# Kernel optimization log

Measured on AMD Instinct MI355X. Metric: run time of the kernel, lower is better.

Reference implementation:

```python
import jax, jax.numpy as jnp
import numpy as np

EPS = 1e-10


def setup_inputs() -> dict:
    key = jax.random.key(0)
    k1, k2 = jax.random.split(key)
    B, C, H, W = 8, 16, 256, 256
    x = jax.random.normal(k1, (B, C, H, W), dtype=jnp.float32)
    # grid_sample-style normalized coords in [-1, 1]
    inv_grid = jax.random.uniform(k2, (B, H, W, 2), dtype=jnp.float32, minval=-1.0, maxval=1.0)
    return {"x": x, "inv_grid": inv_grid}


def reference(x, inv_grid):
    B, C, Hin, Win = x.shape
    h, w = Hin, Win  # OH = OW = None -> output size equals input size

    g = (inv_grid + 1.0) * 0.5
    # coord 0 scaled by h, coord 1 by w, shifted by +1 (padding row/col), clamped
    ci = jnp.clip(g[..., 0] * h + 1.0, 0.0, h + 1 - 2 * EPS)
    cj = jnp.clip(g[..., 1] * w + 1.0, 0.0, w + 1 - 2 * EPS)
    i0 = jnp.floor(ci).astype(jnp.int32)  # coords >= 0 so floor == trunc (.long())
    j0 = jnp.floor(cj).astype(jnp.int32)

    # broadcast over channel dim (grid is shared across channels)
    ci_ = ci[:, None]
    cj_ = cj[:, None]
    i0_ = i0[:, None]
    j0_ = j0[:, None]

    bidx = jnp.arange(B)[:, None, None, None]
    cidx = jnp.arange(C)[None, :, None, None]

    A = jnp.zeros((B, C, h + 3, w + 3), dtype=x.dtype)
    for di in range(2):
        wi = jax.nn.relu(1.0 - jnp.abs(ci_ - (i0_ + di).astype(ci_.dtype)))
        for dj in range(2):
            wj = jax.nn.relu(1.0 - jnp.abs(cj_ - (j0_ + dj).astype(cj_.dtype)))
            # bilinear splat scatter-add of x * weight into the 4 corner cells
            A = A.at[bidx, cidx, i0_ + di, j0_ + dj].add(x * (wi * wj))
    return A[..., 1:h + 1, 1:w + 1]
```

## Files before the change

### kernel.cpp

```cpp
#include <hip/hip_runtime.h>
#include <hip/hip_fp16.h>
#include <stdint.h>

#define BB 8
#define CC 16
#define HH 256
#define WW 256
#define HW (HH * WW)
#define NSRC (BB * HW)
#define NBLK (NSRC / 256)
#define MAXSLOT 15
#define CNT_BYTES ((size_t)NSRC * 4)


__global__ __launch_bounds__(256) void pass1_bin(
    const float* __restrict__ inv_grid,
    uint32_t* __restrict__ counts,
    uint2* __restrict__ srcs)
{
    const int idx = blockIdx.x * 256 + threadIdx.x;
    const float2 g2 = ((const float2*)inv_grid)[idx];
    const float ci = fminf(fmaxf(fmaf((g2.x + 1.0f) * 0.5f, (float)HH, 1.0f), 0.0f), 257.0f);
    const float cj = fminf(fmaxf(fmaf((g2.y + 1.0f) * 0.5f, (float)WW, 1.0f), 0.0f), 257.0f);
    const int i0 = (int)floorf(ci);
    const int j0 = (int)floorf(cj);
    const float fi = ci - (float)i0;
    const float fj = cj - (float)j0;
    const int bi = i0 - 1, bj = j0 - 1;
    uint32_t meta = 0xFFFFFFFFu;
    if (((unsigned)bi < HH) & ((unsigned)bj < WW)) {
        const int b = idx >> 16;
        const uint32_t bin = (b << 16) | (bi << 8) | bj;
        const uint32_t slot = atomicAdd(&counts[bin], 1u);
        if (slot < MAXSLOT) meta = (bin << 4) | slot;
    }
    const uint32_t fi16 = (uint32_t)(fi * 65535.0f + 0.5f);
    const uint32_t fj16 = (uint32_t)(fj * 65535.0f + 0.5f);
    uint2 m; m.x = meta; m.y = fi16 | (fj16 << 16);
    srcs[idx] = m;
}

__global__ __launch_bounds__(256) void scanA(
    const uint32_t* __restrict__ counts,
    uint2* __restrict__ co,
    uint32_t* __restrict__ bsum)
{
    __shared__ uint32_t s[256];
    const int t = threadIdx.x;
    const int i = blockIdx.x * 256 + t;
    const uint32_t v = counts[i];
    s[t] = v;
    __syncthreads();
#pragma unroll
    for (int d = 1; d < 256; d <<= 1) {
        const uint32_t u = (t >= d) ? s[t - d] : 0u;
        __syncthreads();
        s[t] += u;
        __syncthreads();
    }
    uint2 e; e.x = v; e.y = s[t] - v;
    co[i] = e;
    if (t == 255) bsum[blockIdx.x] = s[255];
}

__global__ __launch_bounds__(1024) void scanB(uint32_t* __restrict__ bsum)
{
    __shared__ uint32_t s[1024];
    const int t = threadIdx.x;
    const uint32_t a  = bsum[2 * t];
    const uint32_t b2 = bsum[2 * t + 1];
    const uint32_t pair = a + b2;
    s[t] = pair;
    __syncthreads();
#pragma unroll
    for (int d = 1; d < 1024; d <<= 1) {
        const uint32_t u = (t >= d) ? s[t - d] : 0u;
        __syncthreads();
        s[t] += u;
        __syncthreads();
    }
    const uint32_t excl = s[t] - pair;
    bsum[2 * t]     = excl;
    bsum[2 * t + 1] = excl + a;
}

__global__ __launch_bounds__(256) void fill_records(
    const float* __restrict__ x,
    const uint2* __restrict__ srcs,
    const uint2* __restrict__ co,
    const uint32_t* __restrict__ bsum,
    uint32_t* __restrict__ ff,
    uint4* __restrict__ pl)
{
    const int idx = blockIdx.x * 256 + threadIdx.x;
    const uint2 m = srcs[idx];
    if (m.x == 0xFFFFFFFFu) return;
    const uint32_t bin  = m.x >> 4;
    const uint32_t slot = m.x & 15u;
    const uint32_t pos  = co[bin].y + bsum[bin >> 8] + slot;

    const int b = idx >> 16;
    const int p = idx & 0xFFFF;
    const float* xp = x + (((size_t)b * CC) << 16) + p;

    uint32_t h[8];
#pragma unroll
    for (int q = 0; q < 8; ++q) {
        const float v0 = xp[(size_t)(2 * q)     << 16];
        const float v1 = xp[(size_t)(2 * q + 1) << 16];
        const uint32_t h0 = (uint32_t)__half_as_ushort(__float2half_rn(v0));
        const uint32_t h1 = (uint32_t)__half_as_ushort(__float2half_rn(v1));
        h[q] = h0 | (h1 << 16);
    }
    ff[pos] = m.y;
    uint4 q0; q0.x = h[0]; q0.y = h[1]; q0.z = h[2]; q0.w = h[3];
    uint4 q1; q1.x = h[4]; q1.y = h[5]; q1.z = h[6]; q1.w = h[7];
    pl[(size_t)pos * 2]     = q0;
    pl[(size_t)pos * 2 + 1] = q1;
}

__global__ __launch_bounds__(256) void gather_csr(
    const uint2* __restrict__ co,
    const uint32_t* __restrict__ bsum,
    const uint32_t* __restrict__ ff,
    const uint4* __restrict__ pl,
    float* __restrict__ out)
{
    const int g   = blockIdx.x;
    const int b   = g & 7;
    const int seq = g >> 3;
    const int r   = ((seq >> 4) << 4) + (threadIdx.x >> 4);
    const int c   = ((seq & 15) << 4) + (threadIdx.x & 15);

    float acc[CC];
#pragma unroll
    for (int q = 0; q < CC; ++q) acc[q] = 0.0f;

#pragma unroll
    for (int di = 0; di < 2; ++di) {
        const int i0c = r + di;
        if (i0c < 1) continue;
#pragma unroll
        for (int dj = 0; dj < 2; ++dj) {
            const int j0c = c + dj;
            if (j0c < 1) continue;
            const uint32_t bin = (b << 16) | ((i0c - 1) << 8) | (j0c - 1);
            const uint2 e = co[bin];
            uint32_t cnt = e.x;
            if (cnt > MAXSLOT) cnt = MAXSLOT;
            const uint32_t off = e.y + bsum[bin >> 8];
            for (uint32_t k = 0; k < cnt; ++k) {
                const size_t pos = (size_t)(off + k);
                const uint32_t f2 = ff[pos];
                const float fi = (float)(f2 & 0xFFFFu) * (1.0f / 65535.0f);
                const float fj = (float)(f2 >> 16)     * (1.0f / 65535.0f);
                const float wi = di ? (1.0f - fi) : fi;
                const float wj = dj ? (1.0f - fj) : fj;
                const float w = wi * wj;
                const uint4 q0 = pl[pos * 2];
                const uint4 q1 = pl[pos * 2 + 1];
                const uint32_t hs[8] = {q0.x, q0.y, q0.z, q0.w, q1.x, q1.y, q1.z, q1.w};
#pragma unroll
                for (int q = 0; q < 8; ++q) {
                    const float v0 = __half2float(__ushort_as_half((unsigned short)(hs[q] & 0xFFFFu)));
                    const float v1 = __half2float(__ushort_as_half((unsigned short)(hs[q] >> 16)));
                    acc[2 * q]     += w * v0;
                    acc[2 * q + 1] += w * v1;
                }
            }
        }
    }

    float* op = out + (((size_t)(b * CC)) << 16) + (r << 8) + c;
#pragma unroll
    for (int q = 0; q < CC; ++q)
        op[(size_t)q << 16] = acc[q];
}

__global__ __launch_bounds__(256) void invgrid_scatter_direct(
    const float* __restrict__ x,
    const float* __restrict__ inv_grid,
    float* __restrict__ out)
{
    const int idx = blockIdx.x * 256 + threadIdx.x;
    const int b = idx >> 16;
    const float2 g2 = ((const float2*)inv_grid)[idx];
    const float ci = fminf(fmaxf(fmaf((g2.x + 1.0f) * 0.5f, (float)HH, 1.0f), 0.0f), 257.0f);
    const float cj = fminf(fmaxf(fmaf((g2.y + 1.0f) * 0.5f, (float)WW, 1.0f), 0.0f), 257.0f);
    const int i0 = (int)floorf(ci);
    const int j0 = (int)floorf(cj);
    const float wi0 = fmaxf(0.0f, 1.0f - fabsf(ci - (float)i0));
    const float wi1 = fmaxf(0.0f, 1.0f - fabsf(ci - (float)(i0 + 1)));
    const float wj0 = fmaxf(0.0f, 1.0f - fabsf(cj - (float)j0));
    const float wj1 = fmaxf(0.0f, 1.0f - fabsf(cj - (float)(j0 + 1)));
    const float w00 = wi0 * wj0, w01 = wi0 * wj1;
    const float w10 = wi1 * wj0, w11 = wi1 * wj1;
    const int r0 = i0 - 1, r1 = i0, c0 = j0 - 1, c1 = j0;
    const bool vr0 = (unsigned)r0 < HH, vr1 = (unsigned)r1 < HH;
    const bool vc0 = (unsigned)c0 < WW, vc1 = (unsigned)c1 < WW;
    const int o00 = r0 * WW + c0, o01 = r0 * WW + c1;
    const int o10 = r1 * WW + c0, o11 = r1 * WW + c1;
    const int p = idx & 0xFFFF;
    const float* xp = x + (size_t)b * CC * HW + p;
    float* op = out + (size_t)b * CC * HW;
#pragma unroll
    for (int cch = 0; cch < CC; ++cch) {
        const float xv = xp[(size_t)cch * HW];
        float* ob = op + (size_t)cch * HW;
        if (vr0 & vc0) atomicAdd(ob + o00, xv * w00);
        if (vr0 & vc1) atomicAdd(ob + o01, xv * w01);
        if (vr1 & vc0) atomicAdd(ob + o10, xv * w10);
        if (vr1 & vc1) atomicAdd(ob + o11, xv * w11);
    }
}

extern "C" void kernel_launch(void* const* d_in, const int* in_sizes, int n_in,
                              void* d_out, int out_size, void* d_ws, size_t ws_size,
                              hipStream_t stream) {
    const float* x        = (const float*)d_in[0];
    const float* inv_grid = (const float*)d_in[1];
    float* out            = (float*)d_out;

    const size_t A = 256;
    size_t o_counts = 0;
    size_t o_co     = o_counts + (CNT_BYTES + A - 1) / A * A;
    size_t o_bsum   = o_co     + ((size_t)NSRC * 8 + A - 1) / A * A;
    size_t o_srcs   = o_bsum   + ((size_t)NBLK * 4 + A - 1) / A * A;
    size_t o_ff     = o_srcs   + ((size_t)NSRC * 8 + A - 1) / A * A;
    size_t o_pl     = o_ff     + (CNT_BYTES + A - 1) / A * A;
    size_t need     = o_pl     + (size_t)NSRC * 32;

    if (ws_size >= need) {
        char* w = (char*)d_ws;
        uint32_t* counts = (uint32_t*)(w + o_counts);
        uint2*    co     = (uint2*)   (w + o_co);
        uint32_t* bsum   = (uint32_t*)(w + o_bsum);
        uint2*    srcs   = (uint2*)   (w + o_srcs);
        uint32_t* ff     = (uint32_t*)(w + o_ff);
        uint4*    pl     = (uint4*)   (w + o_pl);
        hipMemsetAsync(counts, 0, CNT_BYTES, stream);
        pass1_bin   <<<NBLK, 256,  0, stream>>>(inv_grid, counts, srcs);
        scanA       <<<NBLK, 256,  0, stream>>>(counts, co, bsum);
        scanB       <<<1,    1024, 0, stream>>>(bsum);
        fill_records<<<NBLK, 256,  0, stream>>>(x, srcs, co, bsum, ff, pl);
        gather_csr  <<<NBLK, 256,  0, stream>>>(co, bsum, ff, pl, out);
    } else {
        hipMemsetAsync(d_out, 0, (size_t)out_size * sizeof(float), stream);
        invgrid_scatter_direct<<<NBLK, 256, 0, stream>>>(x, inv_grid, out);
    }
}
```

Measured before the change: 155.8 us.

## Replace two-level scan with atomic-cursor wave scan and flatten gather loop

The block-wide shared-memory scan plus the single-block scanB kernel are replaced by a wavefront shuffle scan whose block base comes from an atomicAdd on a global cursor, which removes one kernel launch. Each bin's offset and count are packed into one 32-bit word, halving the co array and dropping the bsum lookups. Bins end up in nondeterministic order, but each bin stays contiguous, so the result is unaffected. The gather kernel now walks the four neighbour bins as one flattened, 2-way unrolled loop rather than four nested variable-length loops, to reduce divergence and loop overhead.

```diff
diff --git a/kernel.cpp b/kernel.cpp
--- a/kernel.cpp
+++ b/kernel.cpp
@@ -42,53 +42,43 @@
 
 __global__ __launch_bounds__(256) void scanA(
     const uint32_t* __restrict__ counts,
-    uint2* __restrict__ co,
-    uint32_t* __restrict__ bsum)
-{
-    __shared__ uint32_t s[256];
-    const int t = threadIdx.x;
-    const int i = blockIdx.x * 256 + t;
+    uint32_t* __restrict__ co,
+    uint32_t* __restrict__ cursor)
+{
+    const int t    = threadIdx.x;
+    const int lane = t & 63;
+    const int wv   = t >> 6;
+    const int i    = blockIdx.x * 256 + t;
     const uint32_t v = counts[i];
-    s[t] = v;
+
+    uint32_t s = v;
+#pragma unroll
+    for (int d = 1; d < 64; d <<= 1) {
+        const uint32_t u = __shfl_up(s, (unsigned)d, 64);
+        if (lane >= d) s += u;
+    }
+
+    __shared__ uint32_t wsum[4];
+    __shared__ uint32_t gbase_s;
+    if (lane == 63) wsum[wv] = s;
     __syncthreads();
-#pragma unroll
-    for (int d = 1; d < 256; d <<= 1) {
-        const uint32_t u = (t >= d) ? s[t - d] : 0u;
-        __syncthreads();
-        s[t] += u;
-        __syncthreads();
-    }
-    uint2 e; e.x = v; e.y = s[t] - v;
-    co[i] = e;
-    if (t == 255) bsum[blockIdx.x] = s[255];
-}
-
-__global__ __launch_bounds__(1024) void scanB(uint32_t* __restrict__ bsum)
-{
-    __shared__ uint32_t s[1024];
-    const int t = threadIdx.x;
-    const uint32_t a  = bsum[2 * t];
-    const uint32_t b2 = bsum[2 * t + 1];
-    const uint32_t pair = a + b2;
-    s[t] = pair;
+
+    uint32_t base = 0;
+#pragma unroll
+    for (int w = 0; w < 3; ++w)
+        if (w < wv) base += wsum[w];
+
+    if (t == 255) gbase_s = atomicAdd(cursor, base + s);
     __syncthreads();
-#pragma unroll
-    for (int d = 1; d < 1024; d <<= 1) {
-        const uint32_t u = (t >= d) ? s[t - d] : 0u;
-        __syncthreads();
-        s[t] += u;
-        __syncthreads();
-    }
-    const uint32_t excl = s[t] - pair;
-    bsum[2 * t]     = excl;
-    bsum[2 * t + 1] = excl + a;
+
+    const uint32_t excl = base + s - v + gbase_s;
+    co[i] = (excl << 4) | min(v, 15u);
 }
 
 __global__ __launch_bounds__(256) void fill_records(
     const float* __restrict__ x,
     const uint2* __restrict__ srcs,
-    const uint2* __restrict__ co,
-    const uint32_t* __restrict__ bsum,
+    const uint32_t* __restrict__ co,
     uint32_t* __restrict__ ff,
     uint4* __restrict__ pl)
 {
@@ -97,7 +87,7 @@
     if (m.x == 0xFFFFFFFFu) return;
     const uint32_t bin  = m.x >> 4;
     const uint32_t slot = m.x & 15u;
-    const uint32_t pos  = co[bin].y + bsum[bin >> 8] + slot;
+    const uint32_t pos  = (co[bin] >> 4) + slot;
 
     const int b = idx >> 16;
     const int p = idx & 0xFFFF;
@@ -120,8 +110,7 @@
 }
 
 __global__ __launch_bounds__(256) void gather_csr(
-    const uint2* __restrict__ co,
-    const uint32_t* __restrict__ bsum,
+    const uint32_t* __restrict__ co,
     const uint32_t* __restrict__ ff,
     const uint4* __restrict__ pl,
     float* __restrict__ out)
@@ -132,44 +121,53 @@
     const int r   = ((seq >> 4) << 4) + (threadIdx.x >> 4);
     const int c   = ((seq & 15) << 4) + (threadIdx.x & 15);
 
+    uint32_t cnt[4], off[4];
+#pragma unroll
+    for (int q = 0; q < 4; ++q) {
+        const int row = r + (q >> 1) - 1;
+        const int col = c + (q & 1) - 1;
+        const bool val = (row >= 0) & (col >= 0);
+        const uint32_t rr = val ? (uint32_t)row : 0u;
+        const uint32_t ccol = val ? (uint32_t)col : 0u;
+        const uint32_t bin = ((uint32_t)b << 16) | (rr << 8) | ccol;
+        const uint32_t m = co[bin];
+        cnt[q] = val ? (m & 15u) : 0u;
+        off[q] = m >> 4;
+    }
+    const uint32_t e0 = cnt[0];
+    const uint32_t e1 = e0 + cnt[1];
+    const uint32_t e2 = e1 + cnt[2];
+    const uint32_t T  = e2 + cnt[3];
+
     float acc[CC];
 #pragma unroll
     for (int q = 0; q < CC; ++q) acc[q] = 0.0f;
 
-#pragma unroll
-    for (int di = 0; di < 2; ++di) {
-        const int i0c = r + di;
-        if (i0c < 1) continue;
-#pragma unroll
-        for (int dj = 0; dj < 2; ++dj) {
-            const int j0c = c + dj;
-            if (j0c < 1) continue;
-            const uint32_t bin = (b << 16) | ((i0c - 1) << 8) | (j0c - 1);
-            const uint2 e = co[bin];
-            uint32_t cnt = e.x;
-            if (cnt > MAXSLOT) cnt = MAXSLOT;
-            const uint32_t off = e.y + bsum[bin >> 8];
-            for (uint32_t k = 0; k < cnt; ++k) {
-                const size_t pos = (size_t)(off + k);
-                const uint32_t f2 = ff[pos];
-                const float fi = (float)(f2 & 0xFFFFu) * (1.0f / 65535.0f);
-                const float fj = (float)(f2 >> 16)     * (1.0f / 65535.0f);
-                const float wi = di ? (1.0f - fi) : fi;
-                const float wj = dj ? (1.0f - fj) : fj;
-                const float w = wi * wj;
-                const uint4 q0 = pl[pos * 2];
-                const uint4 q1 = pl[pos * 2 + 1];
-                const uint32_t hs[8] = {q0.x, q0.y, q0.z, q0.w, q1.x, q1.y, q1.z, q1.w};
-#pragma unroll
-                for (int q = 0; q < 8; ++q) {
-                    const float v0 = __half2float(__ushort_as_half((unsigned short)(hs[q] & 0xFFFFu)));
-                    const float v1 = __half2float(__ushort_as_half((unsigned short)(hs[q] >> 16)));
-                    acc[2 * q]     += w * v0;
-                    acc[2 * q + 1] += w * v1;
-                }
-            }
+    auto body = [&](uint32_t t) {
+        const int q = (int)(t >= e0) + (int)(t >= e1) + (int)(t >= e2);
+        const uint32_t base = (q == 0) ? 0u : ((q == 1) ? e0 : ((q == 2) ? e1 : e2));
+        const uint32_t pos = off[q] + (t - base);
+        const uint32_t f2 = ff[pos];
+        const uint4 p0 = pl[(size_t)pos * 2];
+        const uint4 p1 = pl[(size_t)pos * 2 + 1];
+        const float fi = (float)(f2 & 0xFFFFu) * (1.0f / 65535.0f);
+        const float fj = (float)(f2 >> 16)     * (1.0f / 65535.0f);
+        const float wi = (q & 2) ? (1.0f - fi) : fi;
+        const float wj = (q & 1) ? (1.0f - fj) : fj;
+        const float w = wi * wj;
+        const uint32_t hs[8] = {p0.x, p0.y, p0.z, p0.w, p1.x, p1.y, p1.z, p1.w};
+#pragma unroll
+        for (int qq = 0; qq < 8; ++qq) {
+            const float v0 = __half2float(__ushort_as_half((unsigned short)(hs[qq] & 0xFFFFu)));
+            const float v1 = __half2float(__ushort_as_half((unsigned short)(hs[qq] >> 16)));
+            acc[2 * qq]     += w * v0;
+            acc[2 * qq + 1] += w * v1;
         }
-    }
+    };
+
+    uint32_t t = 0;
+    for (; t + 2 <= T; t += 2) { body(t); body(t + 1); }
+    if (t < T) body(t);
 
     float* op = out + (((size_t)(b * CC)) << 16) + (r << 8) + c;
 #pragma unroll
@@ -223,27 +221,26 @@
 
     const size_t A = 256;
     size_t o_counts = 0;
-    size_t o_co     = o_counts + (CNT_BYTES + A - 1) / A * A;
-    size_t o_bsum   = o_co     + ((size_t)NSRC * 8 + A - 1) / A * A;
-    size_t o_srcs   = o_bsum   + ((size_t)NBLK * 4 + A - 1) / A * A;
-    size_t o_ff     = o_srcs   + ((size_t)NSRC * 8 + A - 1) / A * A;
-    size_t o_pl     = o_ff     + (CNT_BYTES + A - 1) / A * A;
-    size_t need     = o_pl     + (size_t)NSRC * 32;
+    size_t o_cursor = CNT_BYTES;
+    size_t o_co     = (CNT_BYTES + 256 + A - 1) / A * A;
+    size_t o_srcs   = o_co   + ((size_t)NSRC * 4 + A - 1) / A * A;
+    size_t o_ff     = o_srcs + ((size_t)NSRC * 8 + A - 1) / A * A;
+    size_t o_pl     = o_ff   + (CNT_BYTES + A - 1) / A * A;
+    size_t need     = o_pl   + (size_t)NSRC * 32;
 
     if (ws_size >= need) {
         char* w = (char*)d_ws;
         uint32_t* counts = (uint32_t*)(w + o_counts);
-        uint2*    co     = (uint2*)   (w + o_co);
-        uint32_t* bsum   = (uint32_t*)(w + o_bsum);
+        uint32_t* cursor = (uint32_t*)(w + o_cursor);
+        uint32_t* co     = (uint32_t*)(w + o_co);
         uint2*    srcs   = (uint2*)   (w + o_srcs);
         uint32_t* ff     = (uint32_t*)(w + o_ff);
         uint4*    pl     = (uint4*)   (w + o_pl);
-        hipMemsetAsync(counts, 0, CNT_BYTES, stream);
-        pass1_bin   <<<NBLK, 256,  0, stream>>>(inv_grid, counts, srcs);
-        scanA       <<<NBLK, 256,  0, stream>>>(counts, co, bsum);
-        scanB       <<<1,    1024, 0, stream>>>(bsum);
-        fill_records<<<NBLK, 256,  0, stream>>>(x, srcs, co, bsum, ff, pl);
-        gather_csr  <<<NBLK, 256,  0, stream>>>(co, bsum, ff, pl, out);
+        hipMemsetAsync(w, 0, CNT_BYTES + 256, stream);
+        pass1_bin   <<<NBLK, 256, 0, stream>>>(inv_grid, counts, srcs);
+        scanA       <<<NBLK, 256, 0, stream>>>(counts, co, cursor);
+        fill_records<<<NBLK, 256, 0, stream>>>(x, srcs, co, ff, pl);
+        gather_csr  <<<NBLK, 256, 0, stream>>>(co, ff, pl, out);
     } else {
         hipMemsetAsync(d_out, 0, (size_t)out_size * sizeof(float), stream);
         invgrid_scatter_direct<<<NBLK, 256, 0, stream>>>(x, inv_grid, out);
```

Measured after the change: 165.1 us. 1.06x slower.
